# Performance work log

Measured on AMD Instinct MI355X. Metric: run time of the kernel, lower is better.

## Reference

```python
import jax, jax.numpy as jnp
import numpy as np

N, E, V_IN, HID, U_IN, B, MEM = 50000, 800000, 128, 128, 64, 64, 128
CAT = V_IN + HID + U_IN  # 320 == hidden*2 + u_in
ALPHA = 0.5
EPS = 1e-5


def setup_inputs() -> dict:
    key = jax.random.key(0)
    ks = jax.random.split(key, 12)
    x = jax.random.normal(ks[0], (N, V_IN), dtype=jnp.float32)
    edge_index = jax.random.randint(ks[1], (2, E), 0, N, dtype=jnp.int64)
    edge_attr = jax.random.normal(ks[2], (E, HID), dtype=jnp.float32)
    u = jax.random.normal(ks[3], (B, U_IN), dtype=jnp.float32)
    batch = jnp.sort(jax.random.randint(ks[4], (N,), 0, B, dtype=jnp.int64))
    Mk = jax.random.normal(ks[5], (MEM, CAT), dtype=jnp.float32)
    Mv = jax.random.normal(ks[6], (MEM, CAT), dtype=jnp.float32)
    ln_gamma = jnp.ones((CAT,), dtype=jnp.float32)
    ln_beta = jnp.zeros((CAT,), dtype=jnp.float32)
    W1 = jax.random.normal(ks[7], (CAT, HID), dtype=jnp.float32) * (1.0 / np.sqrt(CAT))
    b1 = jnp.zeros((HID,), dtype=jnp.float32)
    W2 = jax.random.normal(ks[8], (HID, HID), dtype=jnp.float32) * (1.0 / np.sqrt(HID))
    b2 = jnp.zeros((HID,), dtype=jnp.float32)
    return {"x": x, "edge_index": edge_index, "edge_attr": edge_attr, "u": u,
            "batch": batch, "Mk": Mk, "Mv": Mv, "ln_gamma": ln_gamma,
            "ln_beta": ln_beta, "W1": W1, "b1": b1, "W2": W2, "b2": b2}


def reference(x, edge_index, edge_attr, u, batch, Mk, Mv, ln_gamma, ln_beta, W1, b1, W2, b2):
    # scatter_add over destination nodes
    agg = jax.ops.segment_sum(edge_attr, edge_index[1], num_segments=N)  # [N, HID]
    out = jnp.concatenate([x, agg, u[batch]], axis=1)  # [N, CAT]
    # LayerNorm over last dim
    mu = jnp.mean(out, axis=-1, keepdims=True)
    var = jnp.var(out, axis=-1, keepdims=True)
    out = (out - mu) * jax.lax.rsqrt(var + EPS) * ln_gamma + ln_beta
    # External attention: [N,CAT] @ [CAT,MEM] -> softmax over MEM -> @ [MEM,CAT]
    scores = jnp.einsum('nc,mc->nm', out, Mk)
    attn = jax.nn.softmax(scores, axis=-1)
    attn_out = jnp.einsum('nm,mc->nc', attn, Mv)
    out = ALPHA * attn_out + (1.0 - ALPHA) * out
    # MLP
    h = jax.nn.relu(out @ W1 + b1)
    return h @ W2 + b2
```

## Files before the change

### kernel.cpp

```cpp
#include <hip/hip_runtime.h>

#define NN   50000
#define EE   800000
#define VIN  128
#define HIDN 128
#define UIN  64
#define MEMN 128
#define CATN 320
#define LN_EPS 1e-5f
#define SCAN_NB 196

typedef __attribute__((ext_vector_type(8))) short short8;
typedef __attribute__((ext_vector_type(4))) float f32x4;
typedef __attribute__((ext_vector_type(4))) unsigned int uint4v;
typedef __attribute__((ext_vector_type(4))) unsigned short ushort4v;
typedef unsigned short ushort_t;

__device__ inline ushort_t f32_bf16(float f) {
    unsigned u = __float_as_uint(f);
    return (ushort_t)((u + 0x7FFFu + ((u >> 16) & 1u)) >> 16);
}
__device__ inline float bf16_f32(ushort_t h) {
    return __uint_as_float(((unsigned)h) << 16);
}
__device__ inline unsigned pack_hl(float y) {
    unsigned u  = __float_as_uint(y);
    unsigned hi = (u + 0x7FFFu + ((u >> 16) & 1u)) & 0xFFFF0000u;
    float    lo = y - __uint_as_float(hi);
    unsigned v  = __float_as_uint(lo);
    unsigned l16 = ((v + 0x7FFFu + ((v >> 16) & 1u)) >> 16) & 0xFFFFu;
    return hi | l16;
}

__global__ void hist_kernel(const int* __restrict__ edge_dst, int* __restrict__ count)
{
    int gid = blockIdx.x * 256 + threadIdx.x;
    if (gid < EE) atomicAdd(&count[edge_dst[gid]], 1);
}

__global__ void block_sum_kernel(const int* __restrict__ count, int* __restrict__ partials)
{
    __shared__ int s[256];
    const int tid = threadIdx.x;
    const int gid = blockIdx.x * 256 + tid;
    s[tid] = (gid < NN) ? count[gid] : 0;
    __syncthreads();
    for (int off = 128; off >= 1; off >>= 1) {
        if (tid < off) s[tid] += s[tid + off];
        __syncthreads();
    }
    if (tid == 0) partials[blockIdx.x] = s[0];
}

__global__ void scan_partials_kernel(int* __restrict__ partials)
{
    __shared__ int s[256];
    const int tid = threadIdx.x;
    const int v = (tid < SCAN_NB) ? partials[tid] : 0;
    s[tid] = v;
    __syncthreads();
    for (int off = 1; off < 256; off <<= 1) {
        int t = (tid >= off) ? s[tid - off] : 0;
        __syncthreads();
        s[tid] += t;
        __syncthreads();
    }
    if (tid < SCAN_NB) partials[tid] = s[tid] - v;
}

__global__ void make_offsets_kernel(const int* __restrict__ count,
                                    const int* __restrict__ partials,
                                    int* __restrict__ offsets)
{
    __shared__ int s[256];
    const int tid = threadIdx.x;
    const int gid = blockIdx.x * 256 + tid;
    const int v = (gid < NN) ? count[gid] : 0;
    s[tid] = v;
    __syncthreads();
    for (int off = 1; off < 256; off <<= 1) {
        int t = (tid >= off) ? s[tid - off] : 0;
        __syncthreads();
        s[tid] += t;
        __syncthreads();
    }
    if (gid < NN) offsets[gid] = partials[blockIdx.x] + s[tid] - v;
}

__global__ void fill_kernel(const int* __restrict__ edge_dst,
                            const int* __restrict__ offsets,
                            int* __restrict__ cursor,
                            int* __restrict__ bucket)
{
    int gid = blockIdx.x * 256 + threadIdx.x;
    if (gid >= EE) return;
    const int d = edge_dst[gid];
    const int p = atomicAdd(&cursor[d], 1);
    bucket[offsets[d] + p] = gid;
}

__global__ void prep_mk_kernel(const float* __restrict__ Mk,
                               ushort_t* __restrict__ mk_hi, ushort_t* __restrict__ mk_lo)
{
    int i = blockIdx.x * 256 + threadIdx.x;
    if (i < MEMN * CATN) {
        const float f = Mk[i];
        const ushort_t h = f32_bf16(f);
        mk_hi[i] = h;
        mk_lo[i] = f32_bf16(f - bf16_f32(h));
    }
}
__global__ void prep_mvt_kernel(const float* __restrict__ Mv, ushort_t* __restrict__ mv_t)
{
    int i = blockIdx.x * 256 + threadIdx.x;
    if (i < CATN * MEMN) {
        int c = i >> 7, m = i & 127;
        mv_t[i] = f32_bf16(Mv[m * CATN + c]);
    }
}
__global__ void prep_w1t_kernel(const float* __restrict__ W1, ushort_t* __restrict__ w1_t)
{
    int i = blockIdx.x * 256 + threadIdx.x;
    if (i < HIDN * CATN) {
        int n = i / CATN, k = i - n * CATN;
        w1_t[i] = f32_bf16(W1[k * HIDN + n]);
    }
}
__global__ void prep_w2t_kernel(const float* __restrict__ W2, ushort_t* __restrict__ w2_t)
{
    int i = blockIdx.x * 256 + threadIdx.x;
    if (i < HIDN * HIDN) {
        int n = i >> 7, k = i & 127;
        w2_t[i] = f32_bf16(W2[k * HIDN + n]);
    }
}

__global__ __launch_bounds__(256) void gather_ln_kernel(
    const float* __restrict__ edge_attr,
    const int*   __restrict__ bucket,
    const int*   __restrict__ offsets,
    const int*   __restrict__ count,
    const float* __restrict__ x,
    const float* __restrict__ u,
    const int*   __restrict__ batch,
    const float* __restrict__ gamma,
    const float* __restrict__ beta,
    unsigned*    __restrict__ ln_pk)
{
    const int wid  = (blockIdx.x * 256 + threadIdx.x) >> 6;
    const int lane = threadIdx.x & 63;
    if (wid >= NN) return;

    const int start = offsets[wid];
    const int deg   = count[wid];
    const float2* ea2 = reinterpret_cast<const float2*>(edge_attr);
    float2 a = make_float2(0.f, 0.f);
    int i = 0;
    const int d4 = deg & ~3;
    for (; i < d4; i += 4) {
        const int e0 = bucket[start + i];
        const int e1 = bucket[start + i + 1];
        const int e2 = bucket[start + i + 2];
        const int e3 = bucket[start + i + 3];
        const float2 v0 = ea2[(size_t)e0 * 64 + lane];
        const float2 v1 = ea2[(size_t)e1 * 64 + lane];
        const float2 v2 = ea2[(size_t)e2 * 64 + lane];
        const float2 v3 = ea2[(size_t)e3 * 64 + lane];
        a.x += (v0.x + v1.x) + (v2.x + v3.x);
        a.y += (v0.y + v1.y) + (v2.y + v3.y);
    }
    for (; i < deg; ++i) {
        const int e = bucket[start + i];
        const float2 v = ea2[(size_t)e * 64 + lane];
        a.x += v.x;
        a.y += v.y;
    }
    const float2 xv = reinterpret_cast<const float2*>(x)[(size_t)wid * 64 + lane];
    const float  uv = u[batch[wid] * UIN + lane];

    float s = xv.x + xv.y + a.x + a.y + uv;
    float q = xv.x * xv.x + xv.y * xv.y + a.x * a.x + a.y * a.y + uv * uv;
    #pragma unroll
    for (int off = 32; off >= 1; off >>= 1) {
        s += __shfl_xor(s, off);
        q += __shfl_xor(q, off);
    }
    const float mu  = s * (1.0f / CATN);
    const float var = q * (1.0f / CATN) - mu * mu;
    const float rs  = rsqrtf(var + LN_EPS);

    const float2 g0 = reinterpret_cast<const float2*>(gamma)[lane];
    const float2 g1 = reinterpret_cast<const float2*>(gamma)[64 + lane];
    const float  g2 = gamma[256 + lane];
    const float2 t0 = reinterpret_cast<const float2*>(beta)[lane];
    const float2 t1 = reinterpret_cast<const float2*>(beta)[64 + lane];
    const float  t2 = beta[256 + lane];

    unsigned* row = ln_pk + (size_t)wid * CATN;
    uint2 p01, p23;
    p01.x = pack_hl((xv.x - mu) * rs * g0.x + t0.x);
    p01.y = pack_hl((xv.y - mu) * rs * g0.y + t0.y);
    p23.x = pack_hl((a.x - mu) * rs * g1.x + t1.x);
    p23.y = pack_hl((a.y - mu) * rs * g1.y + t1.y);
    reinterpret_cast<uint2*>(row)[lane]       = p01;
    reinterpret_cast<uint2*>(row + 128)[lane] = p23;
    row[256 + lane] = pack_hl((uv - mu) * rs * g2 + t2);
}

#define MSTR 328
#define SSTR 132
#define PSTR 136

__global__ __launch_bounds__(256) void node_mfma_kernel(
    const unsigned* __restrict__ ln_pk,
    const ushort_t* __restrict__ mk_hi,
    const ushort_t* __restrict__ mk_lo,
    const ushort_t* __restrict__ mv_t,
    const ushort_t* __restrict__ w1_t,
    const ushort_t* __restrict__ w2_t,
    const float*    __restrict__ b1,
    const float*    __restrict__ b2,
    float*          __restrict__ out)
{
    __shared__ __align__(16) ushort_t s_lnh[32 * MSTR];
    __shared__ __align__(16) ushort_t s_lnl[32 * MSTR];
    __shared__ __align__(16) float    s_S[32 * SSTR];
    __shared__ __align__(16) ushort_t s_P[32 * PSTR];

    const int tid  = threadIdx.x;
    const int wv   = tid >> 6;
    const int lane = tid & 63;
    const int l15  = lane & 15;
    const int l4   = lane >> 4;
    const int node0 = blockIdx.x * 32;

    const f32x4 zero4 = {0.f, 0.f, 0.f, 0.f};

    for (int j = tid; j < 32 * 80; j += 256) {
        const int nl = j / 80;
        const int c0 = (j - nl * 80) * 4;
        int ng = node0 + nl; ng = (ng < NN) ? ng : (NN - 1);
        const uint4v p = *(const uint4v*)(ln_pk + (size_t)ng * CATN + c0);
        ushort4v h4, l4v;
        h4.x = (ushort_t)(p.x >> 16);  l4v.x = (ushort_t)(p.x & 0xFFFFu);
        h4.y = (ushort_t)(p.y >> 16);  l4v.y = (ushort_t)(p.y & 0xFFFFu);
        h4.z = (ushort_t)(p.z >> 16);  l4v.z = (ushort_t)(p.z & 0xFFFFu);
        h4.w = (ushort_t)(p.w >> 16);  l4v.w = (ushort_t)(p.w & 0xFFFFu);
        *(ushort4v*)(s_lnh + nl * MSTR + c0) = h4;
        *(ushort4v*)(s_lnl + nl * MSTR + c0) = l4v;
    }
    __syncthreads();

    {
        f32x4 acc[2][2];
        #pragma unroll
        for (int mt = 0; mt < 2; ++mt)
            #pragma unroll
            for (int nt = 0; nt < 2; ++nt) acc[mt][nt] = zero4;

        #pragma unroll 2
        for (int kc = 0; kc < 10; ++kc) {
            const int koff = kc * 32 + l4 * 8;
            short8 ah[2], al[2], bh[2], bl[2];
            #pragma unroll
            for (int mt = 0; mt < 2; ++mt) {
                ah[mt] = *(const short8*)(s_lnh + (mt * 16 + l15) * MSTR + koff);
                al[mt] = *(const short8*)(s_lnl + (mt * 16 + l15) * MSTR + koff);
            }
            #pragma unroll
            for (int nt = 0; nt < 2; ++nt) {
                const int mr = (wv * 2 + nt) * 16 + l15;
                bh[nt] = *(const short8*)(mk_hi + (size_t)mr * CATN + koff);
                bl[nt] = *(const short8*)(mk_lo + (size_t)mr * CATN + koff);
            }
            #pragma unroll
            for (int mt = 0; mt < 2; ++mt)
                #pragma unroll
                for (int nt = 0; nt < 2; ++nt) {
                    acc[mt][nt] = __builtin_amdgcn_mfma_f32_16x16x32_bf16(ah[mt], bh[nt], acc[mt][nt], 0, 0, 0);
                    acc[mt][nt] = __builtin_amdgcn_mfma_f32_16x16x32_bf16(ah[mt], bl[nt], acc[mt][nt], 0, 0, 0);
                    acc[mt][nt] = __builtin_amdgcn_mfma_f32_16x16x32_bf16(al[mt], bh[nt], acc[mt][nt], 0, 0, 0);
                }
        }
        #pragma unroll
        for (int mt = 0; mt < 2; ++mt)
            #pragma unroll
            for (int nt = 0; nt < 2; ++nt)
                #pragma unroll
                for (int r = 0; r < 4; ++r)
                    s_S[(mt * 16 + l4 * 4 + r) * SSTR + (wv * 2 + nt) * 16 + l15] = acc[mt][nt][r];
    }
    __syncthreads();

    {
        const int nd = tid >> 3, j = tid & 7;
        const float* row = s_S + nd * SSTR + j * 16;
        float vals[16];
        float mx = -1e30f;
        #pragma unroll
        for (int i = 0; i < 16; ++i) { vals[i] = row[i]; mx = fmaxf(mx, vals[i]); }
        mx = fmaxf(mx, __shfl_xor(mx, 1));
        mx = fmaxf(mx, __shfl_xor(mx, 2));
        mx = fmaxf(mx, __shfl_xor(mx, 4));
        float sm = 0.f;
        #pragma unroll
        for (int i = 0; i < 16; ++i) { vals[i] = __expf(vals[i] - mx); sm += vals[i]; }
        sm += __shfl_xor(sm, 1);
        sm += __shfl_xor(sm, 2);
        sm += __shfl_xor(sm, 4);
        const float inv = 1.f / sm;
        unsigned* prow = (unsigned*)(s_P + nd * PSTR + j * 16);
        #pragma unroll
        for (int i2 = 0; i2 < 8; ++i2) {
            unsigned pk = (unsigned)f32_bf16(vals[2 * i2] * inv) |
                          ((unsigned)f32_bf16(vals[2 * i2 + 1] * inv) << 16);
            prow[i2] = pk;
        }
    }
    __syncthreads();

    {
        f32x4 acc[2][5];
        #pragma unroll
        for (int mt = 0; mt < 2; ++mt)
            #pragma unroll
            for (int nn = 0; nn < 5; ++nn) acc[mt][nn] = zero4;

        #pragma unroll
        for (int kc = 0; kc < 4; ++kc) {
            const int koff = kc * 32 + l4 * 8;
            short8 ap[2];
            #pragma unroll
            for (int mt = 0; mt < 2; ++mt)
                ap[mt] = *(const short8*)(s_P + (mt * 16 + l15) * PSTR + koff);
            short8 bv[5];
            #pragma unroll
            for (int nn = 0; nn < 5; ++nn) {
                const int c = (wv * 5 + nn) * 16 + l15;
                bv[nn] = *(const short8*)(mv_t + (size_t)c * MEMN + koff);
            }
            #pragma unroll
            for (int mt = 0; mt < 2; ++mt)
                #pragma unroll
                for (int nn = 0; nn < 5; ++nn)
                    acc[mt][nn] = __builtin_amdgcn_mfma_f32_16x16x32_bf16(ap[mt], bv[nn], acc[mt][nn], 0, 0, 0);
        }
        #pragma unroll
        for (int mt = 0; mt < 2; ++mt)
            #pragma unroll
            for (int nn = 0; nn < 5; ++nn)
                #pragma unroll
                for (int r = 0; r < 4; ++r) {
                    const int node_l = mt * 16 + l4 * 4 + r;
                    const int c = (wv * 5 + nn) * 16 + l15;
                    const int idx = node_l * MSTR + c;
                    const float lnv = bf16_f32(s_lnh[idx]) + bf16_f32(s_lnl[idx]);
                    s_lnh[idx] = f32_bf16(0.5f * (acc[mt][nn][r] + lnv));
                }
    }
    __syncthreads();

    {
        f32x4 acc[2][2];
        #pragma unroll
        for (int mt = 0; mt < 2; ++mt)
            #pragma unroll
            for (int nt = 0; nt < 2; ++nt) acc[mt][nt] = zero4;

        #pragma unroll 2
        for (int kc = 0; kc < 10; ++kc) {
            const int koff = kc * 32 + l4 * 8;
            short8 am[2], bw[2];
            #pragma unroll
            for (int mt = 0; mt < 2; ++mt)
                am[mt] = *(const short8*)(s_lnh + (mt * 16 + l15) * MSTR + koff);
            #pragma unroll
            for (int nt = 0; nt < 2; ++nt) {
                const int n = (wv * 2 + nt) * 16 + l15;
                bw[nt] = *(const short8*)(w1_t + (size_t)n * CATN + koff);
            }
            #pragma unroll
            for (int mt = 0; mt < 2; ++mt)
                #pragma unroll
                for (int nt = 0; nt < 2; ++nt)
                    acc[mt][nt] = __builtin_amdgcn_mfma_f32_16x16x32_bf16(am[mt], bw[nt], acc[mt][nt], 0, 0, 0);
        }
        float bb[2];
        #pragma unroll
        for (int nt = 0; nt < 2; ++nt) bb[nt] = b1[(wv * 2 + nt) * 16 + l15];
        __syncthreads();
        #pragma unroll
        for (int mt = 0; mt < 2; ++mt)
            #pragma unroll
            for (int nt = 0; nt < 2; ++nt)
                #pragma unroll
                for (int r = 0; r < 4; ++r) {
                    const int node_l = mt * 16 + l4 * 4 + r;
                    const int col = (wv * 2 + nt) * 16 + l15;
                    s_P[node_l * PSTR + col] = f32_bf16(fmaxf(acc[mt][nt][r] + bb[nt], 0.f));
                }
    }
    __syncthreads();

    {
        f32x4 acc[2][2];
        #pragma unroll
        for (int mt = 0; mt < 2; ++mt)
            #pragma unroll
            for (int nt = 0; nt < 2; ++nt) acc[mt][nt] = zero4;

        #pragma unroll
        for (int kc = 0; kc < 4; ++kc) {
            const int koff = kc * 32 + l4 * 8;
            short8 ah[2], bw[2];
            #pragma unroll
            for (int mt = 0; mt < 2; ++mt)
                ah[mt] = *(const short8*)(s_P + (mt * 16 + l15) * PSTR + koff);
            #pragma unroll
            for (int nt = 0; nt < 2; ++nt) {
                const int n = (wv * 2 + nt) * 16 + l15;
                bw[nt] = *(const short8*)(w2_t + (size_t)n * HIDN + koff);
            }
            #pragma unroll
            for (int mt = 0; mt < 2; ++mt)
                #pragma unroll
                for (int nt = 0; nt < 2; ++nt)
                    acc[mt][nt] = __builtin_amdgcn_mfma_f32_16x16x32_bf16(ah[mt], bw[nt], acc[mt][nt], 0, 0, 0);
        }
        float bb[2];
        #pragma unroll
        for (int nt = 0; nt < 2; ++nt) bb[nt] = b2[(wv * 2 + nt) * 16 + l15];
        #pragma unroll
        for (int mt = 0; mt < 2; ++mt)
            #pragma unroll
            for (int nt = 0; nt < 2; ++nt)
                #pragma unroll
                for (int r = 0; r < 4; ++r) {
                    const int ng = node0 + mt * 16 + l4 * 4 + r;
                    if (ng < NN) {
                        const int col = (wv * 2 + nt) * 16 + l15;
                        out[(size_t)ng * HIDN + col] = acc[mt][nt][r] + bb[nt];
                    }
                }
    }
}

extern "C" void kernel_launch(void* const* d_in, const int* in_sizes, int n_in,
                              void* d_out, int out_size, void* d_ws, size_t ws_size,
                              hipStream_t stream)
{
    const float* x         = (const float*)d_in[0];
    const int*   edge_idx  = (const int*)  d_in[1];
    const float* edge_attr = (const float*)d_in[2];
    const float* u         = (const float*)d_in[3];
    const int*   batch     = (const int*)  d_in[4];
    const float* Mk        = (const float*)d_in[5];
    const float* Mv        = (const float*)d_in[6];
    const float* gamma     = (const float*)d_in[7];
    const float* beta      = (const float*)d_in[8];
    const float* W1        = (const float*)d_in[9];
    const float* b1        = (const float*)d_in[10];
    const float* W2        = (const float*)d_in[11];
    const float* b2        = (const float*)d_in[12];
    float*       out       = (float*)d_out;

    char* w = (char*)d_ws;
    int*   count     = (int*)w;        w += (size_t)NN * sizeof(int);
    int*   cursor    = (int*)w;        w += (size_t)NN * sizeof(int);
    int*   offsets   = (int*)w;        w += (size_t)NN * sizeof(int);
    int*   partials  = (int*)w;        w += 256 * sizeof(int);
    int*   bucket    = (int*)w;        w += (size_t)EE * sizeof(int);
    w = (char*)(((size_t)w + 255) & ~(size_t)255);
    unsigned* ln_pk  = (unsigned*)w;   w += (size_t)NN * CATN * sizeof(unsigned);
    ushort_t* mk_hi  = (ushort_t*)w;   w += (size_t)MEMN * CATN * 2;
    ushort_t* mk_lo  = (ushort_t*)w;   w += (size_t)MEMN * CATN * 2;
    ushort_t* mv_t   = (ushort_t*)w;   w += (size_t)CATN * MEMN * 2;
    ushort_t* w1_t   = (ushort_t*)w;   w += (size_t)HIDN * CATN * 2;
    ushort_t* w2_t   = (ushort_t*)w;   w += (size_t)HIDN * HIDN * 2;

    const int* edge_dst = edge_idx + EE;

    hipMemsetAsync(count, 0, (size_t)2 * NN * sizeof(int), stream);

    const int eb = (EE + 255) / 256;
    hist_kernel<<<eb, 256, 0, stream>>>(edge_dst, count);
    block_sum_kernel<<<SCAN_NB, 256, 0, stream>>>(count, partials);
    scan_partials_kernel<<<1, 256, 0, stream>>>(partials);
    make_offsets_kernel<<<SCAN_NB, 256, 0, stream>>>(count, partials, offsets);
    fill_kernel<<<eb, 256, 0, stream>>>(edge_dst, offsets, cursor, bucket);

    prep_mk_kernel <<<(MEMN * CATN + 255) / 256, 256, 0, stream>>>(Mk, mk_hi, mk_lo);
    prep_mvt_kernel<<<(CATN * MEMN + 255) / 256, 256, 0, stream>>>(Mv, mv_t);
    prep_w1t_kernel<<<(HIDN * CATN + 255) / 256, 256, 0, stream>>>(W1, w1_t);
    prep_w2t_kernel<<<(HIDN * HIDN + 255) / 256, 256, 0, stream>>>(W2, w2_t);

    gather_ln_kernel<<<(NN * 64 + 255) / 256, 256, 0, stream>>>(
        edge_attr, bucket, offsets, count, x, u, batch, gamma, beta, ln_pk);

    node_mfma_kernel<<<(NN + 31) / 32, 256, 0, stream>>>(
        ln_pk, mk_hi, mk_lo, mv_t, w1_t, w2_t, b1, b2, out);
}
```

Before: 311.1 us.

## Compute scores transposed and fuse softmax into MFMA registers

Swaps the MFMA operand roles so the score tile is laid out with memory slots along the accumulator rows and nodes along lanes. Softmax max and sum are then reduced in registers with cross-lane shuffles, and per-wave partials are combined through a small shared buffer. This removes the fp32 score staging array and its store and reload. The cost is that exp is computed twice per element, and the P tile is now written as scattered 16-bit stores that may cause LDS bank conflicts.

```diff
diff --git a/kernel.cpp b/kernel.cpp
--- a/kernel.cpp
+++ b/kernel.cpp
@@ -208,7 +208,6 @@
 }
 
 #define MSTR 328
-#define SSTR 132
 #define PSTR 136
 
 __global__ __launch_bounds__(256) void node_mfma_kernel(
@@ -224,8 +223,8 @@
 {
     __shared__ __align__(16) ushort_t s_lnh[32 * MSTR];
     __shared__ __align__(16) ushort_t s_lnl[32 * MSTR];
-    __shared__ __align__(16) float    s_S[32 * SSTR];
     __shared__ __align__(16) ushort_t s_P[32 * PSTR];
+    __shared__ __align__(16) float2   s_part[8 * 16];
 
     const int tid  = threadIdx.x;
     const int wv   = tid >> 6;
@@ -254,67 +253,70 @@
     {
         f32x4 acc[2][2];
         #pragma unroll
-        for (int mt = 0; mt < 2; ++mt)
-            #pragma unroll
-            for (int nt = 0; nt < 2; ++nt) acc[mt][nt] = zero4;
+        for (int ai = 0; ai < 2; ++ai)
+            #pragma unroll
+            for (int bt = 0; bt < 2; ++bt) acc[ai][bt] = zero4;
 
         #pragma unroll 2
         for (int kc = 0; kc < 10; ++kc) {
             const int koff = kc * 32 + l4 * 8;
-            short8 ah[2], al[2], bh[2], bl[2];
-            #pragma unroll
-            for (int mt = 0; mt < 2; ++mt) {
-                ah[mt] = *(const short8*)(s_lnh + (mt * 16 + l15) * MSTR + koff);
-                al[mt] = *(const short8*)(s_lnl + (mt * 16 + l15) * MSTR + koff);
+            short8 amh[2], aml[2], bnh[2], bnl[2];
+            #pragma unroll
+            for (int ai = 0; ai < 2; ++ai) {
+                const int mr = (wv * 2 + ai) * 16 + l15;
+                amh[ai] = *(const short8*)(mk_hi + (size_t)mr * CATN + koff);
+                aml[ai] = *(const short8*)(mk_lo + (size_t)mr * CATN + koff);
             }
             #pragma unroll
-            for (int nt = 0; nt < 2; ++nt) {
-                const int mr = (wv * 2 + nt) * 16 + l15;
-                bh[nt] = *(const short8*)(mk_hi + (size_t)mr * CATN + koff);
-                bl[nt] = *(const short8*)(mk_lo + (size_t)mr * CATN + koff);
+            for (int bt = 0; bt < 2; ++bt) {
+                bnh[bt] = *(const short8*)(s_lnh + (bt * 16 + l15) * MSTR + koff);
+                bnl[bt] = *(const short8*)(s_lnl + (bt * 16 + l15) * MSTR + koff);
             }
             #pragma unroll
-            for (int mt = 0; mt < 2; ++mt)
-                #pragma unroll
-                for (int nt = 0; nt < 2; ++nt) {
-                    acc[mt][nt] = __builtin_amdgcn_mfma_f32_16x16x32_bf16(ah[mt], bh[nt], acc[mt][nt], 0, 0, 0);
-                    acc[mt][nt] = __builtin_amdgcn_mfma_f32_16x16x32_bf16(ah[mt], bl[nt], acc[mt][nt], 0, 0, 0);
-                    acc[mt][nt] = __builtin_amdgcn_mfma_f32_16x16x32_bf16(al[mt], bh[nt], acc[mt][nt], 0, 0, 0);
+            for (int ai = 0; ai < 2; ++ai)
+                #pragma unroll
+                for (int bt = 0; bt < 2; ++bt) {
+                    acc[ai][bt] = __builtin_amdgcn_mfma_f32_16x16x32_bf16(amh[ai], bnh[bt], acc[ai][bt], 0, 0, 0);
+                    acc[ai][bt] = __builtin_amdgcn_mfma_f32_16x16x32_bf16(aml[ai], bnh[bt], acc[ai][bt], 0, 0, 0);
+                    acc[ai][bt] = __builtin_amdgcn_mfma_f32_16x16x32_bf16(amh[ai], bnl[bt], acc[ai][bt], 0, 0, 0);
                 }
         }
-        #pragma unroll
-        for (int mt = 0; mt < 2; ++mt)
-            #pragma unroll
-            for (int nt = 0; nt < 2; ++nt)
+
+        #pragma unroll
+        for (int bt = 0; bt < 2; ++bt) {
+            float mx = acc[0][bt][0];
+            #pragma unroll
+            for (int ai = 0; ai < 2; ++ai)
+                #pragma unroll
+                for (int r = 0; r < 4; ++r) mx = fmaxf(mx, acc[ai][bt][r]);
+            mx = fmaxf(mx, __shfl_xor(mx, 16));
+            mx = fmaxf(mx, __shfl_xor(mx, 32));
+            float sm = 0.f;
+            #pragma unroll
+            for (int ai = 0; ai < 2; ++ai)
+                #pragma unroll
+                for (int r = 0; r < 4; ++r) sm += __expf(acc[ai][bt][r] - mx);
+            sm += __shfl_xor(sm, 16);
+            sm += __shfl_xor(sm, 32);
+            if (l4 == 0) s_part[(wv * 2 + bt) * 16 + l15] = make_float2(mx, sm);
+        }
+        __syncthreads();
+        #pragma unroll
+        for (int bt = 0; bt < 2; ++bt) {
+            const float2 p0 = s_part[(0 * 2 + bt) * 16 + l15];
+            const float2 p1 = s_part[(1 * 2 + bt) * 16 + l15];
+            const float2 p2 = s_part[(2 * 2 + bt) * 16 + l15];
+            const float2 p3 = s_part[(3 * 2 + bt) * 16 + l15];
+            const float mg = fmaxf(fmaxf(p0.x, p1.x), fmaxf(p2.x, p3.x));
+            const float sg = p0.y * __expf(p0.x - mg) + p1.y * __expf(p1.x - mg)
+                           + p2.y * __expf(p2.x - mg) + p3.y * __expf(p3.x - mg);
+            const float inv = 1.f / sg;
+            ushort_t* prow = s_P + (bt * 16 + l15) * PSTR + (wv * 2) * 16 + l4 * 4;
+            #pragma unroll
+            for (int ai = 0; ai < 2; ++ai)
                 #pragma unroll
                 for (int r = 0; r < 4; ++r)
-                    s_S[(mt * 16 + l4 * 4 + r) * SSTR + (wv * 2 + nt) * 16 + l15] = acc[mt][nt][r];
-    }
-    __syncthreads();
-
-    {
-        const int nd = tid >> 3, j = tid & 7;
-        const float* row = s_S + nd * SSTR + j * 16;
-        float vals[16];
-        float mx = -1e30f;
-        #pragma unroll
-        for (int i = 0; i < 16; ++i) { vals[i] = row[i]; mx = fmaxf(mx, vals[i]); }
-        mx = fmaxf(mx, __shfl_xor(mx, 1));
-        mx = fmaxf(mx, __shfl_xor(mx, 2));
-        mx = fmaxf(mx, __shfl_xor(mx, 4));
-        float sm = 0.f;
-        #pragma unroll
-        for (int i = 0; i < 16; ++i) { vals[i] = __expf(vals[i] - mx); sm += vals[i]; }
-        sm += __shfl_xor(sm, 1);
-        sm += __shfl_xor(sm, 2);
-        sm += __shfl_xor(sm, 4);
-        const float inv = 1.f / sm;
-        unsigned* prow = (unsigned*)(s_P + nd * PSTR + j * 16);
-        #pragma unroll
-        for (int i2 = 0; i2 < 8; ++i2) {
-            unsigned pk = (unsigned)f32_bf16(vals[2 * i2] * inv) |
-                          ((unsigned)f32_bf16(vals[2 * i2 + 1] * inv) << 16);
-            prow[i2] = pk;
+                    prow[ai * 16 + r] = f32_bf16(__expf(acc[ai][bt][r] - mg) * inv);
         }
     }
     __syncthreads();
```

New measurement: 300.8 us. 3.3% less time.
